# Kernel optimization log

Hardware: AMD Instinct MI355X
Metric: run time of the kernel (lower is better)

Reference implementation:

```python
import jax, jax.numpy as jnp
import numpy as np

K = 10  # kNN neighbors (module default)


def _safe_norm(x):
    # norm along last axis with zero (not NaN) gradient at x == 0
    sq = jnp.sum(x * x, axis=-1)
    safe = jnp.where(sq > 0, sq, 1.0)
    return jnp.where(sq > 0, jnp.sqrt(safe), 0.0)


def _angle(v1, v2):
    cross = jnp.cross(v1, v2, axis=-1)
    dot = jnp.sum(v1 * v2, axis=-1)
    return jnp.arctan2(_safe_norm(cross), dot)


def _compute_normals(p, k):
    # squared pairwise distances (same kNN ordering as cdist, cheaper/safer)
    sq = jnp.sum((p[:, None, :] - p[None, :, :]) ** 2, axis=-1)  # (N,N)
    _, knn = jax.lax.top_k(-sq, k + 1)
    knn = knn[:, 1:]                        # drop self, (N,k)
    neigh = p[knn]                          # (N,k,3)
    centered = neigh - neigh.mean(axis=1, keepdims=True)
    cov = jnp.einsum('nki,nkj->nij', centered, centered) / k  # (N,3,3)
    _, eigvecs = jnp.linalg.eigh(cov)
    return eigvecs[:, :, 0]                 # smallest-eigenvalue eigenvector, (N,3)


def reference(points, W, b):
    p = points[0]                           # (N,3)
    n = _compute_normals(p, K)              # (N,3)
    d = p[:, None, :] - p[None, :, :]       # (N,N,3), d[i,j] = p_i - p_j
    ni = jnp.broadcast_to(n[:, None, :], d.shape)
    nj = jnp.broadcast_to(n[None, :, :], d.shape)
    ppf = jnp.stack([
        _safe_norm(d),
        _angle(ni, d),
        _angle(nj, d),
        _angle(ni, nj),
    ], axis=-1)                             # (N,N,4)
    feat = ppf.mean(axis=1)                 # (N,4)
    s = feat @ W.T + b                      # (N,out)
    return s[None]                          # (1,N,out)


def setup_inputs() -> dict:
    key = jax.random.key(0)
    k1, k2 = jax.random.split(key)
    N, OUT = 2048, 256
    points = jax.random.normal(k1, (1, N, 3), dtype=jnp.float32)
    W = jax.random.normal(k2, (OUT, 4), dtype=jnp.float32) * 0.1
    b = jnp.zeros((OUT,), dtype=jnp.float32)
    return {"points": points, "W": W, "b": b}
```

## Files before the change

### kernel.cpp

```cpp
#include <hip/hip_runtime.h>
#include <math.h>

#pragma clang fp contract(off)

#define NPTS 2048
#define KNN 10
#define NOUT 256


__device__ __forceinline__ float lapy2f(float x, float y) {
  float xa = fabsf(x), ya = fabsf(y);
  float w = fmaxf(xa, ya), z = fminf(xa, ya);
  if (z == 0.f) return w;
  float t = z / w;
  return w * sqrtf(1.f + t * t);
}

__device__ __forceinline__ void slartgf(float f, float g, float& c, float& s, float& r) {
  if (g == 0.f) { c = 1.f; s = 0.f; r = f; }
  else if (f == 0.f) { c = 0.f; s = copysignf(1.f, g); r = fabsf(g); }
  else {
    float d = sqrtf(f * f + g * g);
    float p = 1.f / d;
    c = fabsf(f) * p;
    s = g * copysignf(p, f);
    r = copysignf(d, f);
  }
}

__device__ __forceinline__ void slaev2f(float a, float b, float c,
                                        float& rt1, float& rt2, float& cs1, float& sn1) {
  float sm = a + c;
  float df = a - c;
  float adf = fabsf(df);
  float tb = b + b;
  float ab = fabsf(tb);
  float acmx, acmn;
  if (fabsf(a) > fabsf(c)) { acmx = a; acmn = c; } else { acmx = c; acmn = a; }
  float rt;
  if (adf > ab)      { float t = ab / adf; rt = adf * sqrtf(1.f + t * t); }
  else if (adf < ab) { float t = adf / ab; rt = ab * sqrtf(1.f + t * t); }
  else               { rt = ab * sqrtf(2.f); }
  int sgn1;
  if (sm < 0.f) {
    rt1 = 0.5f * (sm - rt); sgn1 = -1;
    rt2 = (acmx / rt1) * acmn - (b / rt1) * b;
  } else if (sm > 0.f) {
    rt1 = 0.5f * (sm + rt); sgn1 = 1;
    rt2 = (acmx / rt1) * acmn - (b / rt1) * b;
  } else {
    rt1 = 0.5f * rt; rt2 = -0.5f * rt; sgn1 = 1;
  }
  int sgn2; float cs;
  if (df >= 0.f) { cs = df + rt; sgn2 = 1; } else { cs = df - rt; sgn2 = -1; }
  float acs = fabsf(cs);
  if (acs > ab) {
    float ct = -tb / cs;
    sn1 = 1.f / sqrtf(1.f + ct * ct);
    cs1 = ct * sn1;
  } else {
    if (ab == 0.f) { cs1 = 1.f; sn1 = 0.f; }
    else {
      float tn = -cs / tb;
      cs1 = 1.f / sqrtf(1.f + tn * tn);
      sn1 = tn * cs1;
    }
  }
  if (sgn1 == sgn2) { float tn = cs1; cs1 = -sn1; sn1 = tn; }
}

#define ROT12(c, s) {                                         \
    float t_;                                                 \
    t_ = z01; z01 = (c) * t_ - (s) * z00; z00 = (s) * t_ + (c) * z00; \
    t_ = z11; z11 = (c) * t_ - (s) * z10; z10 = (s) * t_ + (c) * z10; \
    t_ = z21; z21 = (c) * t_ - (s) * z20; z20 = (s) * t_ + (c) * z20; }
#define ROT23(c, s) {                                         \
    float t_;                                                 \
    t_ = z02; z02 = (c) * t_ - (s) * z01; z01 = (s) * t_ + (c) * z01; \
    t_ = z12; z12 = (c) * t_ - (s) * z11; z11 = (s) * t_ + (c) * z11; \
    t_ = z22; z22 = (c) * t_ - (s) * z21; z21 = (s) * t_ + (c) * z21; }

__device__ __forceinline__ void ssteqr3_reg(
    float& d0, float& d1, float& d2, float& e0, float& e1,
    float& z00, float& z01, float& z02,
    float& z10, float& z11, float& z12,
    float& z20, float& z21, float& z22) {
  const float eps = 5.9604645e-8f;
  const float eps2 = eps * eps;
  const float safmin = 1.1754944e-38f;
  const int nmaxit = 90;
  int jtot = 0;
  int l1 = 1;
  for (int og = 0; og < 4; ++og) {
    if (l1 > 3) break;
    if (l1 == 2) e0 = 0.f;
    else if (l1 == 3) e1 = 0.f;
    int m = 3;
    if (l1 == 1) {
      float t = fabsf(e0);
      if (t == 0.f) m = 1;
      else if (t <= (sqrtf(fabsf(d0)) * sqrtf(fabsf(d1))) * eps) { e0 = 0.f; m = 1; }
      else {
        float t2 = fabsf(e1);
        if (t2 == 0.f) m = 2;
        else if (t2 <= (sqrtf(fabsf(d1)) * sqrtf(fabsf(d2))) * eps) { e1 = 0.f; m = 2; }
      }
    } else if (l1 == 2) {
      float t = fabsf(e1);
      if (t == 0.f) m = 2;
      else if (t <= (sqrtf(fabsf(d1)) * sqrtf(fabsf(d2))) * eps) { e1 = 0.f; m = 2; }
    }
    int l = l1, lend = m;
    l1 = m + 1;
    if (lend == l) continue;
    {
      float dlend = (lend == 1) ? d0 : ((lend == 2) ? d1 : d2);
      float dl = (l == 1) ? d0 : ((l == 2) ? d1 : d2);
      if (fabsf(dlend) < fabsf(dl)) { int t = lend; lend = l; l = t; }
    }
    if (lend > l) {
      for (int it = 0; it < 128; ++it) {
        int m2 = lend;
        if (l != lend) {
          for (int mm = l; mm <= lend - 1; ++mm) {
            float em  = (mm == 1) ? e0 : e1;
            float dm1 = (mm == 1) ? d0 : d1;
            float dm  = (mm == 1) ? d1 : d2;
            float tst = em * em;
            if (tst <= (eps2 * fabsf(dm1)) * fabsf(dm) + safmin) { m2 = mm; break; }
          }
        }
        if (m2 < lend) { if (m2 == 1) e0 = 0.f; else e1 = 0.f; }
        float p = (l == 1) ? d0 : ((l == 2) ? d1 : d2);
        if (m2 == l) { l += 1; if (l <= lend) continue; break; }
        if (m2 == l + 1) {
          float rt1, rt2, c, s;
          if (l == 1) {
            slaev2f(d0, e0, d1, rt1, rt2, c, s);
            ROT12(c, s)
            d0 = rt1; d1 = rt2; e0 = 0.f;
          } else {
            slaev2f(d1, e1, d2, rt1, rt2, c, s);
            ROT23(c, s)
            d1 = rt1; d2 = rt2; e1 = 0.f;
          }
          l += 2; if (l <= lend) continue; break;
        }
        if (jtot == nmaxit) break;
        jtot++;
        float g = (d1 - p) / (2.f * e0);
        float r = lapy2f(g, 1.f);
        g = d2 - p + e0 / (g + copysignf(r, g));
        float s = 1.f, c = 1.f;
        p = 0.f;
        float c0, s0n, c1, s1n;
        {
          float f = s * e1;
          float bb = c * e1;
          slartgf(g, f, c, s, r);
          g = d2 - p;
          r = (d1 - g) * s + 2.f * c * bb;
          p = s * r;
          d2 = g + p;
          g = c * r - bb;
          c1 = c; s1n = -s;
        }
        {
          float f = s * e0;
          float bb = c * e0;
          slartgf(g, f, c, s, r);
          e1 = r;
          g = d1 - p;
          r = (d0 - g) * s + 2.f * c * bb;
          p = s * r;
          d1 = g + p;
          g = c * r - bb;
          c0 = c; s0n = -s;
        }
        ROT23(c1, s1n)
        ROT12(c0, s0n)
        d0 = d0 - p;
        e0 = g;
      }
    } else {
      for (int it = 0; it < 128; ++it) {
        int m2 = lend;
        if (l != lend) {
          for (int mm = l; mm >= lend + 1; --mm) {
            float em  = (mm == 3) ? e1 : e0;
            float dm1 = (mm == 3) ? d2 : d1;
            float dm2 = (mm == 3) ? d1 : d0;
            float tst = em * em;
            if (tst <= (eps2 * fabsf(dm1)) * fabsf(dm2) + safmin) { m2 = mm; break; }
          }
        }
        if (m2 > lend) { if (m2 == 3) e1 = 0.f; else e0 = 0.f; }
        float p = (l == 1) ? d0 : ((l == 2) ? d1 : d2);
        if (m2 == l) { l -= 1; if (l >= lend) continue; break; }
        if (m2 == l - 1) {
          float rt1, rt2, c, s;
          if (l == 2) {
            slaev2f(d0, e0, d1, rt1, rt2, c, s);
            ROT12(c, s)
            d0 = rt1; d1 = rt2; e0 = 0.f;
          } else {
            slaev2f(d1, e1, d2, rt1, rt2, c, s);
            ROT23(c, s)
            d1 = rt1; d2 = rt2; e1 = 0.f;
          }
          l -= 2; if (l >= lend) continue; break;
        }
        if (jtot == nmaxit) break;
        jtot++;
        float g = (d1 - p) / (2.f * e1);
        float r = lapy2f(g, 1.f);
        g = d0 - p + e1 / (g + copysignf(r, g));
        float s = 1.f, c = 1.f;
        p = 0.f;
        float c0, s0p, c1, s1p;
        {
          float f = s * e0;
          float bb = c * e0;
          slartgf(g, f, c, s, r);
          g = d0 - p;
          r = (d1 - g) * s + 2.f * c * bb;
          p = s * r;
          d0 = g + p;
          g = c * r - bb;
          c0 = c; s0p = s;
        }
        {
          float f = s * e1;
          float bb = c * e1;
          slartgf(g, f, c, s, r);
          e0 = r;
          g = d1 - p;
          r = (d2 - g) * s + 2.f * c * bb;
          p = s * r;
          d1 = g + p;
          g = c * r - bb;
          c1 = c; s1p = s;
        }
        ROT12(c0, s0p)
        ROT23(c1, s1p)
        d2 = d2 - p;
        e1 = g;
      }
    }
  }
  {
    int k = 1; float p = d0;
    if (d1 < p) { k = 2; p = d1; }
    if (d2 < p) { k = 3; p = d2; }
    if (k == 2) {
      d1 = d0; d0 = p;
      float t;
      t = z00; z00 = z01; z01 = t;
      t = z10; z10 = z11; z11 = t;
      t = z20; z20 = z21; z21 = t;
    } else if (k == 3) {
      d2 = d0; d0 = p;
      float t;
      t = z00; z00 = z02; z02 = t;
      t = z10; z10 = z12; z12 = t;
      t = z20; z20 = z22; z22 = t;
    }
    k = 2; p = d1;
    if (d2 < p) { k = 3; p = d2; }
    if (k == 3) {
      d2 = d1; d1 = p;
      float t;
      t = z01; z01 = z02; z02 = t;
      t = z11; z11 = z12; z12 = t;
      t = z21; z21 = z22; z22 = t;
    }
  }
}


__global__ __launch_bounds__(256) void knn_normals_kernel(
    const float* __restrict__ pts,
    float* __restrict__ pxa, float* __restrict__ pya, float* __restrict__ pza,
    float* __restrict__ nxa, float* __restrict__ nya, float* __restrict__ nza) {
  __shared__ unsigned long long cand[4 * (KNN + 1)];
  __shared__ int knn_sh[KNN];
  const int tid = threadIdx.x;
  const int lane = tid & 63;
  const int wv = tid >> 6;
  const int p = blockIdx.x;

  {
    float px = pts[3 * p], py = pts[3 * p + 1], pz = pts[3 * p + 2];
    if (tid == 0) { pxa[p] = px; pya[p] = py; pza[p] = pz; }

    unsigned long long k0[8];
#pragma unroll
    for (int t = 0; t < 8; ++t) {
      int j = wv * 512 + t * 64 + lane;
      float dx = px - pts[3 * j];
      float dy = py - pts[3 * j + 1];
      float dz = pz - pts[3 * j + 2];
      float sq = dx * dx;
      sq = sq + dy * dy;
      sq = sq + dz * dz;
      k0[t] = (((unsigned long long)__float_as_uint(sq)) << 32) |
              (unsigned int)j;
    }

#define CE(a, b)                                                          \
    {                                                                     \
      unsigned long long lo = k0[a] < k0[b] ? k0[a] : k0[b];              \
      unsigned long long hi = k0[a] < k0[b] ? k0[b] : k0[a];              \
      k0[a] = lo; k0[b] = hi;                                             \
    }
    CE(0, 1) CE(2, 3) CE(4, 5) CE(6, 7)
    CE(0, 2) CE(1, 3) CE(4, 6) CE(5, 7)
    CE(1, 2) CE(5, 6) CE(0, 4) CE(3, 7)
    CE(1, 5) CE(2, 6)
    CE(1, 4) CE(3, 6)
    CE(2, 4) CE(3, 5)
    CE(3, 4)
#undef CE

    for (int r = 0; r < KNN + 1; ++r) {
      unsigned long long m = k0[0];
#pragma unroll
      for (int off = 32; off > 0; off >>= 1) {
        unsigned long long o = __shfl_xor(m, off, 64);
        m = (o < m) ? o : m;
      }
      if (lane == 0) cand[wv * (KNN + 1) + r] = m;
      if (k0[0] == m) {
#pragma unroll
        for (int q = 0; q < 7; ++q) k0[q] = k0[q + 1];
        k0[7] = 0xFFFFFFFFFFFFFFFFULL;
      }
    }
  }
  __syncthreads();

  if (tid < 4 * (KNN + 1)) {
    unsigned long long e = cand[tid];
    int rank = 0;
#pragma unroll
    for (int m = 0; m < 4 * (KNN + 1); ++m) rank += (cand[m] < e) ? 1 : 0;
    if (rank > 0 && rank <= KNN)
      knn_sh[rank - 1] = (int)(unsigned int)(e & 0xFFFFFFFFULL);
  }
  __syncthreads();

  if (tid == 0) {
    float nx[KNN], ny[KNN], nz[KNN];
    float sx = 0.f, sy = 0.f, sz = 0.f;
#pragma unroll
    for (int t = 0; t < KNN; ++t) {
      int j = knn_sh[t];
      nx[t] = pts[3 * j]; ny[t] = pts[3 * j + 1]; nz[t] = pts[3 * j + 2];
      sx = sx + nx[t]; sy = sy + ny[t]; sz = sz + nz[t];
    }
    float mx = sx / 10.f, my = sy / 10.f, mz = sz / 10.f;
    float a11 = 0.f, a21 = 0.f, a31 = 0.f, a22 = 0.f, a32 = 0.f, a33 = 0.f;
#pragma unroll
    for (int t = 0; t < KNN; ++t) {
      float cx = nx[t] - mx, cy = ny[t] - my, cz = nz[t] - mz;
      a11 = a11 + cx * cx;
      a21 = a21 + cy * cx;
      a31 = a31 + cz * cx;
      a22 = a22 + cy * cy;
      a32 = a32 + cz * cy;
      a33 = a33 + cz * cz;
    }
    a11 = a11 / 10.f; a21 = a21 / 10.f; a31 = a31 / 10.f;
    a22 = a22 / 10.f; a32 = a32 / 10.f; a33 = a33 / 10.f;

    float d0, d1, d2, e0, e1, tau1 = 0.f, v2 = 0.f;
    {
      float alpha = a21;
      float xnorm = fabsf(a31);
      if (xnorm == 0.f) {
        tau1 = 0.f; v2 = 0.f;
        d0 = a11; d1 = a22; d2 = a33; e0 = alpha; e1 = a32;
      } else {
        float beta = -copysignf(lapy2f(alpha, xnorm), alpha);
        tau1 = (beta - alpha) / beta;
        v2 = a31 * (1.f / (alpha - beta));
        float y1 = tau1 * a22; y1 = y1 + tau1 * (a32 * v2);
        float y2 = tau1 * a32; y2 = y2 + (tau1 * v2) * a33;
        float dotv = y1; dotv = dotv + y2 * v2;
        float ac = -0.5f * tau1 * dotv;
        y1 = y1 + ac;
        y2 = y2 + ac * v2;
        float t1 = -y1, t2 = -1.f;
        a22 = (a22 + t1) + y1 * t2;
        a32 = (a32 + v2 * t1) + y2 * t2;
        float t1b = -y2, t2b = -v2;
        a33 = (a33 + v2 * t1b) + y2 * t2b;
        d0 = a11; d1 = a22; d2 = a33; e0 = beta; e1 = a32;
      }
    }
    float z00 = 1.f, z01 = 0.f, z02 = 0.f;
    float z10 = 0.f, z11 = 1.f, z12 = 0.f;
    float z20 = 0.f, z21 = 0.f, z22 = 1.f;
    ssteqr3_reg(d0, d1, d2, e0, e1,
                z00, z01, z02, z10, z11, z12, z20, z21, z22);
    if (tau1 != 0.f) {
      float w = tau1 * (z10 + v2 * z20);
      z10 = z10 - w;
      z20 = z20 - v2 * w;
    }
    nxa[p] = z00;
    nya[p] = z10;
    nza[p] = z20;
  }
}


__device__ __forceinline__ float atan2_pos(float y, float x) {
#pragma clang fp contract(fast)
  float axx = fabsf(x);
  float mn = fminf(axx, y), mx = fmaxf(axx, y);
  float a = mn * __builtin_amdgcn_rcpf(mx);
  a = (mx == 0.f) ? 0.f : a;
  float s = a * a;
  float r = a * (0.9998660f +
           s * (-0.3302995f +
           s * (0.1801410f +
           s * (-0.0851330f +
           s * 0.0208351f))));
  r = (y > axx) ? 1.57079632679f - r : r;
  r = (x < 0.f) ? 3.14159265359f - r : r;
  return r;
}

__device__ __forceinline__ float angle3(float ax, float ay, float az,
                                        float bx, float by, float bz) {
#pragma clang fp contract(fast)
  float cx = ay * bz - az * by;
  float cy = az * bx - ax * bz;
  float cz = ax * by - ay * bx;
  float sq = cx * cx + cy * cy + cz * cz;
  float dot = ax * bx + ay * by + az * bz;
  return atan2_pos(__builtin_amdgcn_sqrtf(sq), dot);
}

__global__ __launch_bounds__(256) void ppf_kernel(
    const float* __restrict__ pxa, const float* __restrict__ pya,
    const float* __restrict__ pza, const float* __restrict__ nxa,
    const float* __restrict__ nya, const float* __restrict__ nza,
    const float* __restrict__ Wm, const float* __restrict__ bias,
    float* __restrict__ out) {
#pragma clang fp contract(fast)
  __shared__ float ps[4][4];
  const int tid = threadIdx.x;
  const int lane = tid & 63;
  const int wv = tid >> 6;
  const int i = blockIdx.x;

  float pxi = pxa[i], pyi = pya[i], pzi = pza[i];
  float ax = nxa[i], ay = nya[i], az = nza[i];

  float s0 = 0.f, s1 = 0.f, s2 = 0.f, s3 = 0.f;
#pragma unroll
  for (int it = 0; it < 8; ++it) {
    int j = wv * 512 + it * 64 + lane;
    float dx = pxi - pxa[j];
    float dy = pyi - pya[j];
    float dz = pzi - pza[j];
    float bx = nxa[j], by = nya[j], bz = nza[j];
    float sq = dx * dx + dy * dy + dz * dz;
    s0 += __builtin_amdgcn_sqrtf(sq);
    s1 += angle3(ax, ay, az, dx, dy, dz);
    s2 += angle3(bx, by, bz, dx, dy, dz);
    s3 += angle3(ax, ay, az, bx, by, bz);
  }

#pragma unroll
  for (int off = 1; off < 64; off <<= 1) {
    s0 += __shfl_xor(s0, off, 64);
    s1 += __shfl_xor(s1, off, 64);
    s2 += __shfl_xor(s2, off, 64);
    s3 += __shfl_xor(s3, off, 64);
  }
  if (lane == 0) { ps[wv][0] = s0; ps[wv][1] = s1; ps[wv][2] = s2; ps[wv][3] = s3; }
  __syncthreads();

  const float inv = 1.f / 2048.f;
  float f0 = ((ps[0][0] + ps[1][0]) + (ps[2][0] + ps[3][0])) * inv;
  float f1 = ((ps[0][1] + ps[1][1]) + (ps[2][1] + ps[3][1])) * inv;
  float f2 = ((ps[0][2] + ps[1][2]) + (ps[2][2] + ps[3][2])) * inv;
  float f3 = ((ps[0][3] + ps[1][3]) + (ps[2][3] + ps[3][3])) * inv;

  float4 w = ((const float4*)Wm)[tid];
  float r = (((f0 * w.x + f1 * w.y) + f2 * w.z) + f3 * w.w) + bias[tid];
  out[(size_t)i * NOUT + tid] = r;
}


extern "C" void kernel_launch(void* const* d_in, const int* in_sizes, int n_in,
                              void* d_out, int out_size, void* d_ws, size_t ws_size,
                              hipStream_t stream) {
  const float* pts = (const float*)d_in[0];
  const float* Wm  = (const float*)d_in[1];
  const float* bs  = (const float*)d_in[2];
  float* out = (float*)d_out;

  float* pxa = (float*)d_ws;
  float* pya = pxa + NPTS;
  float* pza = pya + NPTS;
  float* nxa = pza + NPTS;
  float* nya = nxa + NPTS;
  float* nza = nya + NPTS;

  knn_normals_kernel<<<NPTS, 256, 0, stream>>>(pts, pxa, pya, pza, nxa, nya, nza);
  ppf_kernel<<<NPTS, 256, 0, stream>>>(pxa, pya, pza, nxa, nya, nza, Wm, bs, out);
}
```

Measured before the change: 99.44 us.

## Vectorize loads, exclude self in kNN, split 64-bit shuffles, use Lagrange identity for angles

The kNN kernel now loads point coordinates as float4 with each lane owning 8 contiguous points. It drops the self point up front, so only 10 selection rounds are needed, and does the 64-bit min reduction as two 32-bit shuffle passes. The PPF kernel loads positions and normals as float4 and replaces each cross-product norm with sqrt(|a|^2|b|^2 - dot^2), assuming unit normals. This saves ALU work and memory instructions, but the identity can lose precision for near-parallel vectors and changes the lane-to-point mapping.

```diff
diff --git a/kernel.cpp b/kernel.cpp
--- a/kernel.cpp
+++ b/kernel.cpp
@@ -282,7 +282,7 @@
     const float* __restrict__ pts,
     float* __restrict__ pxa, float* __restrict__ pya, float* __restrict__ pza,
     float* __restrict__ nxa, float* __restrict__ nya, float* __restrict__ nza) {
-  __shared__ unsigned long long cand[4 * (KNN + 1)];
+  __shared__ unsigned long long cand[4 * KNN];
   __shared__ int knn_sh[KNN];
   const int tid = threadIdx.x;
   const int lane = tid & 63;
@@ -293,19 +293,39 @@
     float px = pts[3 * p], py = pts[3 * p + 1], pz = pts[3 * p + 2];
     if (tid == 0) { pxa[p] = px; pya[p] = py; pza[p] = pz; }
 
+    const int j0 = wv * 512 + lane * 8;
+    const float4* p4 = (const float4*)(pts + 3 * (wv * 512));
+    float4 a0 = p4[6 * lane + 0];
+    float4 a1 = p4[6 * lane + 1];
+    float4 a2 = p4[6 * lane + 2];
+    float4 a3 = p4[6 * lane + 3];
+    float4 a4 = p4[6 * lane + 4];
+    float4 a5 = p4[6 * lane + 5];
+
     unsigned long long k0[8];
-#pragma unroll
-    for (int t = 0; t < 8; ++t) {
-      int j = wv * 512 + t * 64 + lane;
-      float dx = px - pts[3 * j];
-      float dy = py - pts[3 * j + 1];
-      float dz = pz - pts[3 * j + 2];
-      float sq = dx * dx;
-      sq = sq + dy * dy;
-      sq = sq + dz * dz;
-      k0[t] = (((unsigned long long)__float_as_uint(sq)) << 32) |
-              (unsigned int)j;
-    }
+#define DISTK(t, X, Y, Z)                                                 \
+    {                                                                     \
+      int j = j0 + (t);                                                   \
+      float dx = px - (X);                                                \
+      float dy = py - (Y);                                                \
+      float dz = pz - (Z);                                                \
+      float sq = dx * dx;                                                 \
+      sq = sq + dy * dy;                                                  \
+      sq = sq + dz * dz;                                                  \
+      unsigned long long key =                                            \
+          (((unsigned long long)__float_as_uint(sq)) << 32) |             \
+          (unsigned int)j;                                                \
+      k0[t] = (j == p) ? 0xFFFFFFFFFFFFFFFFULL : key;                     \
+    }
+    DISTK(0, a0.x, a0.y, a0.z)
+    DISTK(1, a0.w, a1.x, a1.y)
+    DISTK(2, a1.z, a1.w, a2.x)
+    DISTK(3, a2.y, a2.z, a2.w)
+    DISTK(4, a3.x, a3.y, a3.z)
+    DISTK(5, a3.w, a4.x, a4.y)
+    DISTK(6, a4.z, a4.w, a5.x)
+    DISTK(7, a5.y, a5.z, a5.w)
+#undef DISTK
 
 #define CE(a, b)                                                          \
     {                                                                     \
@@ -322,15 +342,24 @@
     CE(3, 4)
 #undef CE
 
-    for (int r = 0; r < KNN + 1; ++r) {
-      unsigned long long m = k0[0];
+    for (int r = 0; r < KNN; ++r) {
+      unsigned hi0 = (unsigned)(k0[0] >> 32);
+      unsigned lo0 = (unsigned)(k0[0] & 0xFFFFFFFFULL);
+      unsigned mhi = hi0;
 #pragma unroll
       for (int off = 32; off > 0; off >>= 1) {
-        unsigned long long o = __shfl_xor(m, off, 64);
-        m = (o < m) ? o : m;
-      }
-      if (lane == 0) cand[wv * (KNN + 1) + r] = m;
-      if (k0[0] == m) {
+        unsigned o = __shfl_xor(mhi, off, 64);
+        mhi = o < mhi ? o : mhi;
+      }
+      unsigned mlo = (hi0 == mhi) ? lo0 : 0xFFFFFFFFu;
+#pragma unroll
+      for (int off = 32; off > 0; off >>= 1) {
+        unsigned o = __shfl_xor(mlo, off, 64);
+        mlo = o < mlo ? o : mlo;
+      }
+      if (lane == 0)
+        cand[wv * KNN + r] = (((unsigned long long)mhi) << 32) | mlo;
+      if (hi0 == mhi && lo0 == mlo) {
 #pragma unroll
         for (int q = 0; q < 7; ++q) k0[q] = k0[q + 1];
         k0[7] = 0xFFFFFFFFFFFFFFFFULL;
@@ -339,13 +368,13 @@
   }
   __syncthreads();
 
-  if (tid < 4 * (KNN + 1)) {
+  if (tid < 4 * KNN) {
     unsigned long long e = cand[tid];
     int rank = 0;
 #pragma unroll
-    for (int m = 0; m < 4 * (KNN + 1); ++m) rank += (cand[m] < e) ? 1 : 0;
-    if (rank > 0 && rank <= KNN)
-      knn_sh[rank - 1] = (int)(unsigned int)(e & 0xFFFFFFFFULL);
+    for (int m = 0; m < 4 * KNN; ++m) rank += (cand[m] < e) ? 1 : 0;
+    if (rank < KNN)
+      knn_sh[rank] = (int)(unsigned int)(e & 0xFFFFFFFFULL);
   }
   __syncthreads();
 
@@ -432,17 +461,6 @@
   return r;
 }
 
-__device__ __forceinline__ float angle3(float ax, float ay, float az,
-                                        float bx, float by, float bz) {
-#pragma clang fp contract(fast)
-  float cx = ay * bz - az * by;
-  float cy = az * bx - ax * bz;
-  float cz = ax * by - ay * bx;
-  float sq = cx * cx + cy * cy + cz * cz;
-  float dot = ax * bx + ay * by + az * bz;
-  return atan2_pos(__builtin_amdgcn_sqrtf(sq), dot);
-}
-
 __global__ __launch_bounds__(256) void ppf_kernel(
     const float* __restrict__ pxa, const float* __restrict__ pya,
     const float* __restrict__ pza, const float* __restrict__ nxa,
@@ -461,17 +479,36 @@
 
   float s0 = 0.f, s1 = 0.f, s2 = 0.f, s3 = 0.f;
 #pragma unroll
-  for (int it = 0; it < 8; ++it) {
-    int j = wv * 512 + it * 64 + lane;
-    float dx = pxi - pxa[j];
-    float dy = pyi - pya[j];
-    float dz = pzi - pza[j];
-    float bx = nxa[j], by = nya[j], bz = nza[j];
-    float sq = dx * dx + dy * dy + dz * dz;
-    s0 += __builtin_amdgcn_sqrtf(sq);
-    s1 += angle3(ax, ay, az, dx, dy, dz);
-    s2 += angle3(bx, by, bz, dx, dy, dz);
-    s3 += angle3(ax, ay, az, bx, by, bz);
+  for (int it = 0; it < 2; ++it) {
+    int j0 = wv * 512 + it * 256 + lane * 4;
+    float4 jx = *(const float4*)(pxa + j0);
+    float4 jy = *(const float4*)(pya + j0);
+    float4 jz = *(const float4*)(pza + j0);
+    float4 mx4 = *(const float4*)(nxa + j0);
+    float4 my4 = *(const float4*)(nya + j0);
+    float4 mz4 = *(const float4*)(nza + j0);
+#define PAIR(PX, PY, PZ, BX, BY, BZ)                                      \
+    {                                                                     \
+      float dx = pxi - (PX);                                              \
+      float dy = pyi - (PY);                                              \
+      float dz = pzi - (PZ);                                              \
+      float sq = dx * dx + dy * dy + dz * dz;                             \
+      s0 += __builtin_amdgcn_sqrtf(sq);                                   \
+      float da = ax * dx + ay * dy + az * dz;                             \
+      s1 += atan2_pos(                                                    \
+          __builtin_amdgcn_sqrtf(fmaxf(sq - da * da, 0.f)), da);          \
+      float db = (BX) * dx + (BY) * dy + (BZ) * dz;                       \
+      s2 += atan2_pos(                                                    \
+          __builtin_amdgcn_sqrtf(fmaxf(sq - db * db, 0.f)), db);          \
+      float dn = ax * (BX) + ay * (BY) + az * (BZ);                       \
+      s3 += atan2_pos(                                                    \
+          __builtin_amdgcn_sqrtf(fmaxf(1.f - dn * dn, 0.f)), dn);         \
+    }
+    PAIR(jx.x, jy.x, jz.x, mx4.x, my4.x, mz4.x)
+    PAIR(jx.y, jy.y, jz.y, mx4.y, my4.y, mz4.y)
+    PAIR(jx.z, jy.z, jz.z, mx4.z, my4.z, mz4.z)
+    PAIR(jx.w, jy.w, jz.w, mx4.w, my4.w, mz4.w)
+#undef PAIR
   }
 
 #pragma unroll
```

New measurement: 95.56 us. 1.04x faster.
